# Performance work log

Measured on AMD Instinct MI355X. Metric: run time of the kernel, lower is better.

## Reference

```python
import jax, jax.numpy as jnp
import numpy as np

S = 8192  # sequence length
D = 256   # feature dim


def setup_inputs() -> dict:
    key = jax.random.key(0)
    kq, kk, kv = jax.random.split(key, 3)
    Q = jax.random.normal(kq, (S, D), dtype=jnp.float32)
    K = jax.random.normal(kk, (S, D), dtype=jnp.float32)
    V = jax.random.normal(kv, (S, D), dtype=jnp.float32)
    return {"Q": Q, "K": K, "V": V}


def reference(Q, K, V):
    # Faithful to the torch module: dk = K.size(-2) (the SEQUENCE length, not head dim)
    dk = K.shape[-2]
    scores = (Q @ K.T) / jnp.sqrt(jnp.float32(dk))  # [S, S]
    # F.softmax with implicit dim on a 2D tensor -> softmax over last dim (keys)
    attn = jax.nn.softmax(scores, axis=-1)
    return attn @ V  # [S, D]
```

## Files before the change

### kernel.cpp

```cpp
#include <hip/hip_runtime.h>


typedef __attribute__((ext_vector_type(4))) float    f32x4;
typedef __attribute__((ext_vector_type(8))) short    s16x8;
typedef __attribute__((ext_vector_type(4))) short    s16x4;
typedef __attribute__((ext_vector_type(4))) _Float16 f16x4;

#define SEQ 8192
#define DIM 256
#define NSPLIT 8
#define KPS (SEQ / NSPLIT)
#define BN 32
#define ITERS (KPS / BN)
#define BM 128

#define KSC (1.4426950408889634f / 90.50966799187808f)

static __device__ inline short f2bf(float f) {
    unsigned u = __float_as_uint(f);
    return (short)((u + 0x7FFFu + ((u >> 16) & 1u)) >> 16);
}
static __device__ inline short f2bf_fast(float f) {
    return (short)((__float_as_uint(f) + 0x8000u) >> 16);
}

__global__ void cast_qk(const float* __restrict__ Q, const float* __restrict__ K,
                        short* __restrict__ Qb, short* __restrict__ Kb) {
    int idx = blockIdx.x * 256 + threadIdx.x;
    f32x4 q = ((const f32x4*)Q)[idx];
    f32x4 k = ((const f32x4*)K)[idx];
    s16x4 qo, ko;
    qo.x = f2bf(q.x); qo.y = f2bf(q.y); qo.z = f2bf(q.z); qo.w = f2bf(q.w);
    ko.x = f2bf(k.x); ko.y = f2bf(k.y); ko.z = f2bf(k.z); ko.w = f2bf(k.w);
    ((s16x4*)Qb)[idx] = qo;
    ((s16x4*)Kb)[idx] = ko;
}

__global__ void transpose_v(const float* __restrict__ V, short* __restrict__ Vt) {
    __shared__ short tile[32][264];
    int kt = blockIdx.x, tid = threadIdx.x;
    #pragma unroll
    for (int i = 0; i < 8; ++i) {
        int c = tid + i * 256;
        int row = c >> 6, col = c & 63;
        f32x4 v = ((const f32x4*)V)[(size_t)(kt * 32 + row) * 64 + col];
        tile[row][col * 4 + 0] = f2bf(v.x);
        tile[row][col * 4 + 1] = f2bf(v.y);
        tile[row][col * 4 + 2] = f2bf(v.z);
        tile[row][col * 4 + 3] = f2bf(v.w);
    }
    __syncthreads();
    int d = tid;
    short* dst = Vt + (size_t)kt * 8192 + d * 32;
    #pragma unroll
    for (int k8 = 0; k8 < 4; ++k8) {
        s16x8 w;
        #pragma unroll
        for (int j = 0; j < 8; ++j) w[j] = tile[k8 * 8 + j][d];
        *(s16x8*)(dst + k8 * 8) = w;
    }
}

__global__ void __launch_bounds__(256, 2)
attn(const short* __restrict__ Qb, const short* __restrict__ Kb,
     const short* __restrict__ Vt, _Float16* __restrict__ Op,
     float* __restrict__ lp) {
    __shared__ short K_lds[32][264];
    __shared__ short V_lds[256][40];
    __shared__ short P_lds[4][32][40];

    int tid = threadIdx.x;
    int wid = tid >> 6, lane = tid & 63;
    int l15 = lane & 15, qq = lane >> 4;
    int qt = blockIdx.x >> 3, sp = blockIdx.x & 7;

    int qrow0 = qt * BM + wid * 32;
    s16x8 qf[2][8];
    #pragma unroll
    for (int t = 0; t < 2; ++t) {
        const short* qsrc = Qb + (size_t)(qrow0 + t * 16 + l15) * DIM + qq * 8;
        #pragma unroll
        for (int s = 0; s < 8; ++s) qf[t][s] = *(const s16x8*)(qsrc + s * 32);
    }

    s16x8 of;
    #pragma unroll
    for (int j = 0; j < 8; ++j) of[j] = (l15 == 0) ? (short)0x3F80 : (short)0;

    const short* ksrc = Kb + (size_t)(sp * KPS + (tid >> 5)) * DIM + (tid & 31) * 8;
    const short* vsrc = Vt + (size_t)sp * (KPS / 32) * 8192 + (tid >> 2) * 32 + (tid & 3) * 8;
    short* kdst = &K_lds[tid >> 5][(tid & 31) * 8];
    short* vdst = &V_lds[tid >> 2][(tid & 3) * 8];

    f32x4 acc[2][16] = {};
    f32x4 accl[2] = {};

    for (int it = 0; it < ITERS; ++it) {
        __syncthreads();
        #pragma unroll
        for (int p = 0; p < 4; ++p) {
            *(s16x8*)(kdst + p * 8 * 264) = *(const s16x8*)(ksrc + p * 8 * DIM);
            *(s16x8*)(vdst + p * 64 * 40) = *(const s16x8*)(vsrc + p * 64 * 32);
        }
        ksrc += BN * DIM;
        vsrc += 8192;
        __syncthreads();

        f32x4 sc[2][2] = {};
        #pragma unroll
        for (int s = 0; s < 8; ++s) {
            s16x8 kf0 = *(const s16x8*)&K_lds[l15][s * 32 + qq * 8];
            s16x8 kf1 = *(const s16x8*)&K_lds[16 + l15][s * 32 + qq * 8];
            #pragma unroll
            for (int t = 0; t < 2; ++t) {
                sc[t][0] = __builtin_amdgcn_mfma_f32_16x16x32_bf16(qf[t][s], kf0, sc[t][0], 0, 0, 0);
                sc[t][1] = __builtin_amdgcn_mfma_f32_16x16x32_bf16(qf[t][s], kf1, sc[t][1], 0, 0, 0);
            }
        }

        #pragma unroll
        for (int t = 0; t < 2; ++t)
            #pragma unroll
            for (int r = 0; r < 4; ++r) {
                P_lds[wid][t * 16 + qq * 4 + r][l15]      = f2bf_fast(__builtin_amdgcn_exp2f(sc[t][0][r] * KSC));
                P_lds[wid][t * 16 + qq * 4 + r][16 + l15] = f2bf_fast(__builtin_amdgcn_exp2f(sc[t][1][r] * KSC));
            }
        s16x8 pf0 = *(const s16x8*)&P_lds[wid][l15][qq * 8];
        s16x8 pf1 = *(const s16x8*)&P_lds[wid][16 + l15][qq * 8];

        #pragma unroll
        for (int n = 0; n < 16; ++n) {
            s16x8 vf = *(const s16x8*)&V_lds[n * 16 + l15][qq * 8];
            acc[0][n] = __builtin_amdgcn_mfma_f32_16x16x32_bf16(pf0, vf, acc[0][n], 0, 0, 0);
            acc[1][n] = __builtin_amdgcn_mfma_f32_16x16x32_bf16(pf1, vf, acc[1][n], 0, 0, 0);
        }
        accl[0] = __builtin_amdgcn_mfma_f32_16x16x32_bf16(pf0, of, accl[0], 0, 0, 0);
        accl[1] = __builtin_amdgcn_mfma_f32_16x16x32_bf16(pf1, of, accl[1], 0, 0, 0);
    }

    #pragma unroll
    for (int t = 0; t < 2; ++t) {
        #pragma unroll
        for (int n = 0; n < 16; ++n)
            #pragma unroll
            for (int r = 0; r < 4; ++r) {
                int row = qrow0 + t * 16 + qq * 4 + r;
                Op[((size_t)sp * SEQ + row) * DIM + n * 16 + l15] = (_Float16)acc[t][n][r];
            }
        if (l15 == 0) {
            #pragma unroll
            for (int r = 0; r < 4; ++r)
                lp[(size_t)sp * SEQ + qrow0 + t * 16 + qq * 4 + r] = accl[t][r];
        }
    }
}

__global__ void combine(const _Float16* __restrict__ Op, const float* __restrict__ lp,
                        float* __restrict__ out) {
    int idx = blockIdx.x * 256 + threadIdx.x;
    int row = idx >> 6;
    f32x4 a = {};
    float l = 0.0f;
    #pragma unroll
    for (int s = 0; s < NSPLIT; ++s) {
        f16x4 h = *(const f16x4*)(Op + (size_t)s * SEQ * DIM + (size_t)idx * 4);
        a.x += (float)h.x; a.y += (float)h.y; a.z += (float)h.z; a.w += (float)h.w;
        l += lp[s * SEQ + row];
    }
    float linv = 1.0f / l;
    ((f32x4*)out)[idx] = a * linv;
}

extern "C" void kernel_launch(void* const* d_in, const int* in_sizes, int n_in,
                              void* d_out, int out_size, void* d_ws, size_t ws_size,
                              hipStream_t stream) {
    const float* Q = (const float*)d_in[0];
    const float* K = (const float*)d_in[1];
    const float* V = (const float*)d_in[2];
    float* out = (float*)d_out;

    char* ws = (char*)d_ws;
    short*    Qb = (short*)ws;
    short*    Kb = (short*)(ws + (4u << 20));
    short*    Vt = (short*)(ws + (8u << 20));
    _Float16* Op = (_Float16*)(ws + (12u << 20));
    float*    lp = (float*)(ws + (44u << 20));

    cast_qk    <<<2048, 256, 0, stream>>>(Q, K, Qb, Kb);
    transpose_v<<<256, 256, 0, stream>>>(V, Vt);
    attn       <<<NSPLIT * (SEQ / BM), 256, 0, stream>>>(Qb, Kb, Vt, Op, lp);
    combine    <<<2048, 256, 0, stream>>>(Op, lp, out);
}
```

Measured before the change: 162.1 us.

## Use FP8 QK^T MFMA, merge prep kernels, and pad P LDS layout

Quantizes Q and K to FP8 and computes the score matrix with fp8 MFMA instructions, which halves the Q/K memory and LDS traffic and uses the higher-throughput FP8 matrix path. The Q/K cast and the V transpose are merged into one prep kernel, removing a launch. The P LDS tile is padded differently and read as 32-bit words to reduce bank conflicts. The exponent is clamped to guard against overflow. The trade-off is lower score precision, because the softmax still runs without a max subtraction, so FP8 error in the scores is amplified through the exponential.

```diff
diff --git a/kernel.cpp b/kernel.cpp
--- a/kernel.cpp
+++ b/kernel.cpp
@@ -3,8 +3,10 @@
 
 typedef __attribute__((ext_vector_type(4))) float    f32x4;
 typedef __attribute__((ext_vector_type(8))) short    s16x8;
-typedef __attribute__((ext_vector_type(4))) short    s16x4;
+typedef __attribute__((ext_vector_type(4))) int      i32x4;
 typedef __attribute__((ext_vector_type(4))) _Float16 f16x4;
+typedef int  __attribute__((may_alias)) int_a;
+typedef long __attribute__((may_alias)) long_a;
 
 #define SEQ 8192
 #define DIM 256
@@ -24,72 +26,85 @@
     return (short)((__float_as_uint(f) + 0x8000u) >> 16);
 }
 
-__global__ void cast_qk(const float* __restrict__ Q, const float* __restrict__ K,
-                        short* __restrict__ Qb, short* __restrict__ Kb) {
-    int idx = blockIdx.x * 256 + threadIdx.x;
-    f32x4 q = ((const f32x4*)Q)[idx];
-    f32x4 k = ((const f32x4*)K)[idx];
-    s16x4 qo, ko;
-    qo.x = f2bf(q.x); qo.y = f2bf(q.y); qo.z = f2bf(q.z); qo.w = f2bf(q.w);
-    ko.x = f2bf(k.x); ko.y = f2bf(k.y); ko.z = f2bf(k.z); ko.w = f2bf(k.w);
-    ((s16x4*)Qb)[idx] = qo;
-    ((s16x4*)Kb)[idx] = ko;
-}
-
-__global__ void transpose_v(const float* __restrict__ V, short* __restrict__ Vt) {
+__global__ void __launch_bounds__(256)
+prep(const float* __restrict__ Q, const float* __restrict__ K,
+     const float* __restrict__ V, unsigned char* __restrict__ Q8,
+     unsigned char* __restrict__ K8, short* __restrict__ Vt) {
     __shared__ short tile[32][264];
-    int kt = blockIdx.x, tid = threadIdx.x;
+    int b = blockIdx.x, t = threadIdx.x;
+
+    {
+        int row = b * 32 + (t >> 3);
+        int c0 = (t & 7) * 8;
+        const f32x4* q4 = (const f32x4*)Q + (size_t)row * 64 + c0;
+        const f32x4* k4 = (const f32x4*)K + (size_t)row * 64 + c0;
+        int qo[8], ko[8];
+        #pragma unroll
+        for (int i = 0; i < 8; ++i) {
+            f32x4 q = q4[i], k = k4[i];
+            int dq = 0, dk = 0;
+            dq = __builtin_amdgcn_cvt_pk_fp8_f32(q.x, q.y, dq, false);
+            dq = __builtin_amdgcn_cvt_pk_fp8_f32(q.z, q.w, dq, true);
+            dk = __builtin_amdgcn_cvt_pk_fp8_f32(k.x, k.y, dk, false);
+            dk = __builtin_amdgcn_cvt_pk_fp8_f32(k.z, k.w, dk, true);
+            qo[i] = dq; ko[i] = dk;
+        }
+        i32x4* qd = (i32x4*)(Q8 + (size_t)row * 256 + (t & 7) * 32);
+        i32x4* kd = (i32x4*)(K8 + (size_t)row * 256 + (t & 7) * 32);
+        qd[0] = *(i32x4*)&qo[0]; qd[1] = *(i32x4*)&qo[4];
+        kd[0] = *(i32x4*)&ko[0]; kd[1] = *(i32x4*)&ko[4];
+    }
+
     #pragma unroll
     for (int i = 0; i < 8; ++i) {
-        int c = tid + i * 256;
+        int c = t + i * 256;
         int row = c >> 6, col = c & 63;
-        f32x4 v = ((const f32x4*)V)[(size_t)(kt * 32 + row) * 64 + col];
+        f32x4 v = ((const f32x4*)V)[(size_t)(b * 32 + row) * 64 + col];
         tile[row][col * 4 + 0] = f2bf(v.x);
         tile[row][col * 4 + 1] = f2bf(v.y);
         tile[row][col * 4 + 2] = f2bf(v.z);
         tile[row][col * 4 + 3] = f2bf(v.w);
     }
     __syncthreads();
-    int d = tid;
-    short* dst = Vt + (size_t)kt * 8192 + d * 32;
+    short* dst = Vt + (size_t)b * 8192 + t * 32;
     #pragma unroll
     for (int k8 = 0; k8 < 4; ++k8) {
         s16x8 w;
         #pragma unroll
-        for (int j = 0; j < 8; ++j) w[j] = tile[k8 * 8 + j][d];
+        for (int j = 0; j < 8; ++j) w[j] = tile[k8 * 8 + j][t];
         *(s16x8*)(dst + k8 * 8) = w;
     }
 }
 
 __global__ void __launch_bounds__(256, 2)
-attn(const short* __restrict__ Qb, const short* __restrict__ Kb,
+attn(const unsigned char* __restrict__ Q8, const unsigned char* __restrict__ K8,
      const short* __restrict__ Vt, _Float16* __restrict__ Op,
      float* __restrict__ lp) {
-    __shared__ short K_lds[32][264];
+    __shared__ unsigned char K_lds[32][272];
     __shared__ short V_lds[256][40];
-    __shared__ short P_lds[4][32][40];
+    __shared__ short P_lds[4][32][34];
 
     int tid = threadIdx.x;
     int wid = tid >> 6, lane = tid & 63;
     int l15 = lane & 15, qq = lane >> 4;
     int qt = blockIdx.x >> 3, sp = blockIdx.x & 7;
-
     int qrow0 = qt * BM + wid * 32;
-    s16x8 qf[2][8];
+
+    long qf[2][8];
     #pragma unroll
     for (int t = 0; t < 2; ++t) {
-        const short* qsrc = Qb + (size_t)(qrow0 + t * 16 + l15) * DIM + qq * 8;
-        #pragma unroll
-        for (int s = 0; s < 8; ++s) qf[t][s] = *(const s16x8*)(qsrc + s * 32);
+        const unsigned char* p = Q8 + (size_t)(qrow0 + t * 16 + l15) * DIM + qq * 8;
+        #pragma unroll
+        for (int s = 0; s < 8; ++s) qf[t][s] = *(const long_a*)(p + s * 32);
     }
 
     s16x8 of;
     #pragma unroll
     for (int j = 0; j < 8; ++j) of[j] = (l15 == 0) ? (short)0x3F80 : (short)0;
 
-    const short* ksrc = Kb + (size_t)(sp * KPS + (tid >> 5)) * DIM + (tid & 31) * 8;
-    const short* vsrc = Vt + (size_t)sp * (KPS / 32) * 8192 + (tid >> 2) * 32 + (tid & 3) * 8;
-    short* kdst = &K_lds[tid >> 5][(tid & 31) * 8];
+    const unsigned char* ksrc = K8 + (size_t)(sp * KPS + (tid >> 4)) * DIM + (tid & 15) * 16;
+    unsigned char* kdst = &K_lds[tid >> 4][(tid & 15) * 16];
+    const short* vsrc = Vt + (size_t)sp * (KPS / BN) * 8192 + (tid >> 2) * 32 + (tid & 3) * 8;
     short* vdst = &V_lds[tid >> 2][(tid & 3) * 8];
 
     f32x4 acc[2][16] = {};
@@ -97,11 +112,11 @@
 
     for (int it = 0; it < ITERS; ++it) {
         __syncthreads();
-        #pragma unroll
-        for (int p = 0; p < 4; ++p) {
-            *(s16x8*)(kdst + p * 8 * 264) = *(const s16x8*)(ksrc + p * 8 * DIM);
+        *(i32x4*)kdst              = *(const i32x4*)ksrc;
+        *(i32x4*)(kdst + 16 * 272) = *(const i32x4*)(ksrc + 16 * DIM);
+        #pragma unroll
+        for (int p = 0; p < 4; ++p)
             *(s16x8*)(vdst + p * 64 * 40) = *(const s16x8*)(vsrc + p * 64 * 32);
-        }
         ksrc += BN * DIM;
         vsrc += 8192;
         __syncthreads();
@@ -109,12 +124,12 @@
         f32x4 sc[2][2] = {};
         #pragma unroll
         for (int s = 0; s < 8; ++s) {
-            s16x8 kf0 = *(const s16x8*)&K_lds[l15][s * 32 + qq * 8];
-            s16x8 kf1 = *(const s16x8*)&K_lds[16 + l15][s * 32 + qq * 8];
+            long kf0 = *(const long_a*)&K_lds[l15][s * 32 + qq * 8];
+            long kf1 = *(const long_a*)&K_lds[16 + l15][s * 32 + qq * 8];
             #pragma unroll
             for (int t = 0; t < 2; ++t) {
-                sc[t][0] = __builtin_amdgcn_mfma_f32_16x16x32_bf16(qf[t][s], kf0, sc[t][0], 0, 0, 0);
-                sc[t][1] = __builtin_amdgcn_mfma_f32_16x16x32_bf16(qf[t][s], kf1, sc[t][1], 0, 0, 0);
+                sc[t][0] = __builtin_amdgcn_mfma_f32_16x16x32_fp8_fp8(qf[t][s], kf0, sc[t][0], 0, 0, 0);
+                sc[t][1] = __builtin_amdgcn_mfma_f32_16x16x32_fp8_fp8(qf[t][s], kf1, sc[t][1], 0, 0, 0);
             }
         }
 
@@ -122,20 +137,27 @@
         for (int t = 0; t < 2; ++t)
             #pragma unroll
             for (int r = 0; r < 4; ++r) {
-                P_lds[wid][t * 16 + qq * 4 + r][l15]      = f2bf_fast(__builtin_amdgcn_exp2f(sc[t][0][r] * KSC));
-                P_lds[wid][t * 16 + qq * 4 + r][16 + l15] = f2bf_fast(__builtin_amdgcn_exp2f(sc[t][1][r] * KSC));
+                float e0 = fminf(sc[t][0][r] * KSC, 16.0f);
+                float e1 = fminf(sc[t][1][r] * KSC, 16.0f);
+                P_lds[wid][t * 16 + qq * 4 + r][l15]      = f2bf_fast(__builtin_amdgcn_exp2f(e0));
+                P_lds[wid][t * 16 + qq * 4 + r][16 + l15] = f2bf_fast(__builtin_amdgcn_exp2f(e1));
             }
-        s16x8 pf0 = *(const s16x8*)&P_lds[wid][l15][qq * 8];
-        s16x8 pf1 = *(const s16x8*)&P_lds[wid][16 + l15][qq * 8];
+        const int_a* pb = (const int_a*)&P_lds[wid][0][0];
+        union { int u[4]; s16x8 v; } p0, p1;
+        #pragma unroll
+        for (int w = 0; w < 4; ++w) {
+            p0.u[w] = pb[l15 * 17 + qq * 4 + w];
+            p1.u[w] = pb[(16 + l15) * 17 + qq * 4 + w];
+        }
 
         #pragma unroll
         for (int n = 0; n < 16; ++n) {
             s16x8 vf = *(const s16x8*)&V_lds[n * 16 + l15][qq * 8];
-            acc[0][n] = __builtin_amdgcn_mfma_f32_16x16x32_bf16(pf0, vf, acc[0][n], 0, 0, 0);
-            acc[1][n] = __builtin_amdgcn_mfma_f32_16x16x32_bf16(pf1, vf, acc[1][n], 0, 0, 0);
-        }
-        accl[0] = __builtin_amdgcn_mfma_f32_16x16x32_bf16(pf0, of, accl[0], 0, 0, 0);
-        accl[1] = __builtin_amdgcn_mfma_f32_16x16x32_bf16(pf1, of, accl[1], 0, 0, 0);
+            acc[0][n] = __builtin_amdgcn_mfma_f32_16x16x32_bf16(p0.v, vf, acc[0][n], 0, 0, 0);
+            acc[1][n] = __builtin_amdgcn_mfma_f32_16x16x32_bf16(p1.v, vf, acc[1][n], 0, 0, 0);
+        }
+        accl[0] = __builtin_amdgcn_mfma_f32_16x16x32_bf16(p0.v, of, accl[0], 0, 0, 0);
+        accl[1] = __builtin_amdgcn_mfma_f32_16x16x32_bf16(p1.v, of, accl[1], 0, 0, 0);
     }
 
     #pragma unroll
@@ -167,7 +189,7 @@
         a.x += (float)h.x; a.y += (float)h.y; a.z += (float)h.z; a.w += (float)h.w;
         l += lp[s * SEQ + row];
     }
-    float linv = 1.0f / l;
+    float linv = 1.0f / (l + 1e-20f);
     ((f32x4*)out)[idx] = a * linv;
 }
 
@@ -180,14 +202,13 @@
     float* out = (float*)d_out;
 
     char* ws = (char*)d_ws;
-    short*    Qb = (short*)ws;
-    short*    Kb = (short*)(ws + (4u << 20));
-    short*    Vt = (short*)(ws + (8u << 20));
-    _Float16* Op = (_Float16*)(ws + (12u << 20));
-    float*    lp = (float*)(ws + (44u << 20));
-
-    cast_qk    <<<2048, 256, 0, stream>>>(Q, K, Qb, Kb);
-    transpose_v<<<256, 256, 0, stream>>>(V, Vt);
-    attn       <<<NSPLIT * (SEQ / BM), 256, 0, stream>>>(Qb, Kb, Vt, Op, lp);
-    combine    <<<2048, 256, 0, stream>>>(Op, lp, out);
-}
+    unsigned char* Q8 = (unsigned char*)ws;
+    unsigned char* K8 = (unsigned char*)(ws + (2u << 20));
+    short*    Vt = (short*)(ws + (4u << 20));
+    _Float16* Op = (_Float16*)(ws + (8u << 20));
+    float*    lp = (float*)(ws + (40u << 20));
+
+    prep   <<<256, 256, 0, stream>>>(Q, K, V, Q8, K8, Vt);
+    attn   <<<NSPLIT * (SEQ / BM), 256, 0, stream>>>(Q8, K8, Vt, Op, lp);
+    combine<<<2048, 256, 0, stream>>>(Op, lp, out);
+}
```

Result: faster. 156.7 us (-3.3%).
